# Optimization experiments

Hardware: AMD Instinct MI355X
Metric: run time of the kernel (lower is better)

The kernel has to match this reference:

```python
import jax, jax.numpy as jnp
import numpy as np
import math

B, S, H = 2, 2048, 1024
NH, DK, DV = 16, 64, 64
PAD = 0
VOCAB = 32000


def setup_inputs() -> dict:
    key = jax.random.key(0)
    ks = jax.random.split(key, 6)
    batch = jax.random.normal(ks[0], (B, S, H), dtype=jnp.float32)
    input_ids = jax.random.randint(ks[1], (B, S), 1, VOCAB)
    n_pad = S // 20
    input_ids = input_ids.at[:, S - n_pad:].set(PAD)
    init = 1.0 / math.sqrt(H)  # xavier-ish scale
    W_Q = jax.random.normal(ks[2], (H, NH * DK), dtype=jnp.float32) * init
    W_K = jax.random.normal(ks[3], (H, NH * DK), dtype=jnp.float32) * init
    W_V = jax.random.normal(ks[4], (H, NH * DV), dtype=jnp.float32) * init
    W_O = jax.random.normal(ks[5], (NH * DV, H), dtype=jnp.float32) * init
    return {
        "batch": batch, "input_ids": input_ids,
        "W_Q": W_Q, "W_K": W_K, "W_V": W_V,
        "b_Q": jnp.zeros((NH * DK,), jnp.float32),
        "b_K": jnp.zeros((NH * DK,), jnp.float32),
        "b_V": jnp.zeros((NH * DV,), jnp.float32),
        "W_O": W_O, "b_O": jnp.zeros((H,), jnp.float32),
    }


def reference(batch, input_ids, W_Q, W_K, W_V, b_Q, b_K, b_V, W_O, b_O):
    Bn, Sn, _ = batch.shape
    NEG = jnp.float32(-jnp.inf)
    # causal mask [S,S]: 0 where i>=j else -inf
    i = jnp.arange(Sn)
    causal = jnp.where(i[:, None] >= i[None, :], 0.0, NEG).astype(batch.dtype)
    # padding mask [B,1,S]: -inf at pad key positions
    pad = jnp.where(input_ids == PAD, NEG, 0.0).astype(batch.dtype)
    mask = causal[None, :, :] + pad[:, None, :]  # [B,S,S]

    Q = (batch @ W_Q + b_Q).reshape(Bn, Sn, NH, DK)
    K = (batch @ W_K + b_K).reshape(Bn, Sn, NH, DK)
    V = (batch @ W_V + b_V).reshape(Bn, Sn, NH, DV)

    scores = jnp.einsum('bqhd,bkhd->bhqk', Q, K) / math.sqrt(DK)
    attn = jax.nn.softmax(scores + mask[:, None, :, :], axis=-1)
    out = jnp.einsum('bhqk,bkhd->bqhd', attn, V).reshape(Bn, Sn, NH * DV)
    return out @ W_O + b_O
```

## Files before the change

### kernel.cpp

```cpp
#include <hip/hip_runtime.h>
#include <stdint.h>


typedef unsigned short u16;
typedef __attribute__((ext_vector_type(8))) __bf16 bf16x8;
typedef __attribute__((ext_vector_type(4))) float f32x4;
typedef __attribute__((ext_vector_type(4))) short s16x4;
typedef __attribute__((ext_vector_type(8))) short s16x8;
typedef __attribute__((ext_vector_type(2))) uint32_t u32x2;

#define SCL 0.18033688011112042f

__device__ __forceinline__ u16 f2bf(float f) {
  union { float f; uint32_t u; } v; v.f = f;
  uint32_t r = v.u + 0x7FFFu + ((v.u >> 16) & 1u);
  return (u16)(r >> 16);
}

__device__ __forceinline__ void gl_lds16(const u16* g, u16* l) {
  auto gp = reinterpret_cast<const __attribute__((address_space(1))) uint32_t*>(
      reinterpret_cast<uintptr_t>(g));
  auto lp = reinterpret_cast<__attribute__((address_space(3))) uint32_t*>(
      reinterpret_cast<uintptr_t>(l));
  __builtin_amdgcn_global_load_lds(gp, lp, 16, 0, 0);
}

__global__ void k_prologue(const float* __restrict__ batch, const int* __restrict__ ids,
                           const float* __restrict__ W_Q, const float* __restrict__ W_K,
                           const float* __restrict__ W_V, const float* __restrict__ W_O,
                           u16* __restrict__ Xbf, u16* __restrict__ dqkv, u16* __restrict__ dwo,
                           unsigned long long* __restrict__ pb) {
  __shared__ float tile[32][33];
  const int bx = blockIdx.x, t = threadIdx.x;
  if (bx < 4096) {
    int idx = (bx * 256 + t) * 4;
    const float4 v = *reinterpret_cast<const float4*>(batch + idx);
    uint2 o;
    o.x = (uint32_t)f2bf(v.x) | ((uint32_t)f2bf(v.y) << 16);
    o.y = (uint32_t)f2bf(v.z) | ((uint32_t)f2bf(v.w) << 16);
    *reinterpret_cast<uint2*>(Xbf + idx) = o;
  } else if (bx < 8192) {
    int b2 = bx - 4096;
    int z = b2 >> 10;
    b2 &= 1023;
    const float* src = z == 0 ? W_Q : (z == 1 ? W_K : (z == 2 ? W_V : W_O));
    u16* dst = z < 3 ? dqkv + (size_t)z * 1024 * 1024 : dwo;
    int c0 = (b2 & 31) * 32, r0 = (b2 >> 5) * 32;
    int tx = t & 31, ty = t >> 5;
#pragma unroll
    for (int i = 0; i < 4; ++i)
      tile[ty + i * 8][tx] = src[(size_t)(r0 + ty + i * 8) * 1024 + c0 + tx];
    __syncthreads();
#pragma unroll
    for (int i = 0; i < 4; ++i)
      dst[(size_t)(c0 + ty + i * 8) * 1024 + r0 + tx] = f2bf(tile[tx][ty + i * 8]);
  } else {
    int idx = (bx - 8192) * 4 + (t >> 6);
    int ln = t & 63;
    int b = idx >> 5, j = idx & 31;
    unsigned long long m = __ballot(ids[b * 2048 + j * 64 + ln] == 0);
    if (ln == 0) pb[idx] = m;
  }
}


__device__ __forceinline__ void gemm_tile_acc(
    const u16* __restrict__ A, const u16* __restrict__ Bt, int K,
    int tm, int tn, u16* As0, u16* As1, u16* Bs0, u16* Bs1, f32x4 acc[4][4]) {
  const int t = threadIdx.x, wv = t >> 6, ln = t & 63;
  const int wr = (wv & 1) * 64, wc = (wv >> 1) * 64;
  const int lr = ln & 15, q8 = (ln >> 4) * 8;
  const int srow = ln >> 2, scol = (ln & 3) * 8;

  for (int k0 = 0; k0 < K; k0 += 64) {
#pragma unroll
    for (int i = 0; i < 2; ++i) {
      int c = wv + i * 4;
      const size_t ra = (size_t)(tm + c * 16 + srow) * K + k0 + scol;
      const size_t rb = (size_t)(tn + c * 16 + srow) * K + k0 + scol;
      gl_lds16(A + ra,       As0 + c * 512 + ln * 8);
      gl_lds16(A + ra + 32,  As1 + c * 512 + ln * 8);
      gl_lds16(Bt + rb,      Bs0 + c * 512 + ln * 8);
      gl_lds16(Bt + rb + 32, Bs1 + c * 512 + ln * 8);
    }
    __syncthreads();
#pragma unroll
    for (int s = 0; s < 2; ++s) {
      const u16* Asb = s ? As1 : As0;
      const u16* Bsb = s ? Bs1 : Bs0;
      bf16x8 av[4], bv[4];
#pragma unroll
      for (int m = 0; m < 4; ++m)
        av[m] = *reinterpret_cast<const bf16x8*>(Asb + (wr + m * 16 + lr) * 32 + q8);
#pragma unroll
      for (int n = 0; n < 4; ++n)
        bv[n] = *reinterpret_cast<const bf16x8*>(Bsb + (wc + n * 16 + lr) * 32 + q8);
#pragma unroll
      for (int m = 0; m < 4; ++m)
#pragma unroll
        for (int n = 0; n < 4; ++n)
          acc[m][n] = __builtin_amdgcn_mfma_f32_16x16x32_bf16(av[m], bv[n], acc[m][n], 0, 0, 0);
    }
    __syncthreads();
  }
}

__global__ __launch_bounds__(256) void k_qkv(
    const u16* __restrict__ X, const u16* __restrict__ Wt,
    const float* __restrict__ bQ, const float* __restrict__ bK, const float* __restrict__ bV,
    u16* __restrict__ Qt, u16* __restrict__ Kt, u16* __restrict__ Vt) {
  __shared__ __align__(16) u16 As0[128 * 32];
  __shared__ __align__(16) u16 As1[128 * 32];
  __shared__ __align__(16) u16 Bs0[128 * 32];
  __shared__ __align__(16) u16 Bs1[128 * 32];
  f32x4 acc[4][4] = {};
  const int tm = blockIdx.x * 128, tn = blockIdx.y * 128;
  gemm_tile_acc(X, Wt, 1024, tm, tn, As0, As1, Bs0, Bs1, acc);

  const int t = threadIdx.x, wv = t >> 6, ln = t & 63;
  const int wr = (wv & 1) * 64, wc = (wv >> 1) * 64;
  const int lr = ln & 15, q4 = (ln >> 4) * 4;
  const int which = tn >> 10;

  if (which == 0) {
#pragma unroll
    for (int n = 0; n < 4; ++n) {
      int f = (tn + wc + n * 16 + lr) & 1023;
      float bb = bQ[f];
      int h = f >> 6, dd = f & 63;
      int kh = dd >> 5, qq = (dd & 31) >> 3, e = dd & 7;
#pragma unroll
      for (int m = 0; m < 4; ++m)
#pragma unroll
        for (int r = 0; r < 4; ++r) {
          int gr = tm + wr + m * 16 + q4 + r;
          int b = gr >> 11, s = gr & 2047;
          int bh = b * 16 + h;
          size_t addr = (((size_t)(bh * 64 + (s >> 5)) * 4 + ((s & 31) >> 4) * 2 + kh) << 9) +
                        ((s & 15) + 16 * qq) * 8 + e;
          Qt[addr] = f2bf((acc[m][n][r] + bb) * SCL);
        }
    }
  } else if (which == 1) {
#pragma unroll
    for (int n = 0; n < 4; ++n) {
      int f = (tn + wc + n * 16 + lr) & 1023;
      float bb = bK[f];
      int h = f >> 6, dd = f & 63;
      int kh = dd >> 5, qq = (dd & 31) >> 3, e = dd & 7;
#pragma unroll
      for (int m = 0; m < 4; ++m)
#pragma unroll
        for (int r = 0; r < 4; ++r) {
          int gr = tm + wr + m * 16 + q4 + r;
          int b = gr >> 11, s = gr & 2047;
          int bh = b * 16 + h;
          size_t addr = (((size_t)(bh * 32 + (s >> 6)) * 8 + kh * 4 + ((s & 63) >> 4)) << 9) +
                        ((s & 15) + 16 * qq) * 8 + e;
          Kt[addr] = f2bf(acc[m][n][r] + bb);
        }
    }
  } else {
#pragma unroll
    for (int n = 0; n < 4; ++n) {
      int f = (tn + wc + n * 16 + lr) & 1023;
      float bb = bV[f];
      int h = f >> 6, dd = f & 63;
      int md = dd >> 4, iv = dd & 15;
#pragma unroll
      for (int m = 0; m < 4; ++m) {
        int gr0 = tm + wr + m * 16 + q4;
        int b = gr0 >> 11, s0 = gr0 & 2047;
        int bh = b * 16 + h;
        int j = s0 >> 6, k5 = s0 & 63;
        int mp = k5 >> 5, g = (k5 & 15) >> 2, h0 = (k5 & 16) >> 2;
        size_t addr = (((size_t)(bh * 32 + j) * 8 + mp * 4 + md) << 9) +
                      (g * 16 + iv) * 8 + h0;
        uint2 pk;
        pk.x = (uint32_t)f2bf(acc[m][n][0] + bb) | ((uint32_t)f2bf(acc[m][n][1] + bb) << 16);
        pk.y = (uint32_t)f2bf(acc[m][n][2] + bb) | ((uint32_t)f2bf(acc[m][n][3] + bb) << 16);
        *reinterpret_cast<uint2*>(Vt + addr) = pk;
      }
    }
  }
}

__global__ __launch_bounds__(256) void k_out(
    const u16* __restrict__ O, const u16* __restrict__ WoT,
    const float* __restrict__ bO, float* __restrict__ out) {
  __shared__ __align__(16) u16 As0[128 * 32];
  __shared__ __align__(16) u16 As1[128 * 32];
  __shared__ __align__(16) u16 Bs0[128 * 32];
  __shared__ __align__(16) u16 Bs1[128 * 32];
  f32x4 acc[4][4] = {};
  const int tm = blockIdx.x * 128, tn = blockIdx.y * 128;
  gemm_tile_acc(O, WoT, 1024, tm, tn, As0, As1, Bs0, Bs1, acc);

  const int t = threadIdx.x, wv = t >> 6, ln = t & 63;
  const int wr = (wv & 1) * 64, wc = (wv >> 1) * 64;
  const int lr = ln & 15, q4 = (ln >> 4) * 4;
#pragma unroll
  for (int n = 0; n < 4; ++n) {
    int gc = tn + wc + n * 16 + lr;
    float bb = bO[gc];
#pragma unroll
    for (int m = 0; m < 4; ++m)
#pragma unroll
      for (int r = 0; r < 4; ++r) {
        int gr = tm + wr + m * 16 + q4 + r;
        out[(size_t)gr * 1024 + gc] = acc[m][n][r] + bb;
      }
  }
}

__global__ __launch_bounds__(256, 3) void k_attn(
    const u16* __restrict__ Qt, const u16* __restrict__ Kt, const u16* __restrict__ Vt,
    const unsigned long long* __restrict__ padbits,
    u16* __restrict__ Opart, float* __restrict__ Lpart) {
  __shared__ __align__(16) u16 KsA[2 * 4096];
  __shared__ __align__(16) u16 VsA[2 * 4096];

  const int id = blockIdx.x;
  const int bh = id & 31;
  const int w = 39 - (id >> 5);
  int p, c;
  if (w < 4)       { p = w;                    c = 0; }
  else if (w < 12) { p = 4 + ((w - 4) >> 1);   c = (w - 4) & 1; }
  else if (w < 24) { p = 8 + (w - 12) / 3;     c = (w - 12) % 3; }
  else             { p = 12 + ((w - 24) >> 2); c = (w - 24) & 3; }
  const int jts = c * 8;
  const int jte = min(2 * p + 2, jts + 8);
  const int slot = bh * 40 + w;
  const int bI = bh >> 4;

  const int t = threadIdx.x, wv = t >> 6, ln = t & 63;
  const int lr = ln & 15, q4 = (ln >> 4) * 4;
  const int qbase = p * 128 + wv * 32;
  const int qrow = wv * 32;

  bf16x8 bq[2][2];
  {
    const u16* qb = Qt + (((size_t)(bh * 64 + (qbase >> 5)) * 4) << 9) + ln * 8;
#pragma unroll
    for (int n = 0; n < 2; ++n)
#pragma unroll
      for (int kh = 0; kh < 2; ++kh)
        bq[n][kh] = *reinterpret_cast<const bf16x8*>(qb + ((n * 2 + kh) << 9));
  }

  float lo[2] = {0.f, 0.f};
  f32x4 Oc[4][2] = {};

  const int st = t * 8;
  const u16* kgp = Kt + (((size_t)(bh * 32 + jts)) << 12) + st;
  const u16* vgp = Vt + (((size_t)(bh * 32 + jts)) << 12) + st;

#pragma unroll
  for (int r = 0; r < 2; ++r) {
    gl_lds16(kgp + r * 2048, &KsA[st + r * 2048]);
    gl_lds16(vgp + r * 2048, &VsA[st + r * 2048]);
  }
  __syncthreads();

  int co = 0;
  for (int j = jts; j < jte; ++j) {
    if (j + 1 < jte) {
      kgp += 4096; vgp += 4096;
      const int no = co ^ 4096;
#pragma unroll
      for (int r = 0; r < 2; ++r) {
        gl_lds16(kgp + r * 2048, &KsA[no + st + r * 2048]);
        gl_lds16(vgp + r * 2048, &VsA[no + st + r * 2048]);
      }
    }

    const int kb = j * 64;
    const unsigned long long pb = padbits[bI * 32 + j];
    const bool masked = (kb + 63 > qbase) || (pb != 0);

    f32x4 sc[4][2] = {};
#pragma unroll
    for (int m = 0; m < 4; ++m) {
      const bf16x8 ak0 = *reinterpret_cast<const bf16x8*>(&KsA[co + m * 512 + ln * 8]);
      const bf16x8 ak1 = *reinterpret_cast<const bf16x8*>(&KsA[co + (4 + m) * 512 + ln * 8]);
#pragma unroll
      for (int n = 0; n < 2; ++n) {
        sc[m][n] = __builtin_amdgcn_mfma_f32_16x16x32_bf16(ak0, bq[n][0], sc[m][n], 0, 0, 0);
        sc[m][n] = __builtin_amdgcn_mfma_f32_16x16x32_bf16(ak1, bq[n][1], sc[m][n], 0, 0, 0);
      }
    }

    s16x4 pbf[4][2];
#pragma unroll
    for (int n = 0; n < 2; ++n) {
      if (masked) {
        const int qabs = qbase + n * 16 + lr;
#pragma unroll
        for (int m = 0; m < 4; ++m)
#pragma unroll
          for (int r = 0; r < 4; ++r) {
            const int sl = m * 16 + q4 + r;
            const bool dead = (kb + sl > qabs) || ((pb >> sl) & 1ull);
            sc[m][n][r] = dead ? -1e30f : sc[m][n][r];
          }
      }
      float ps = 0.f;
#pragma unroll
      for (int m = 0; m < 4; ++m) {
        float p0 = __builtin_amdgcn_exp2f(sc[m][n][0]);
        float p1 = __builtin_amdgcn_exp2f(sc[m][n][1]);
        float p2 = __builtin_amdgcn_exp2f(sc[m][n][2]);
        float p3 = __builtin_amdgcn_exp2f(sc[m][n][3]);
        ps += (p0 + p1) + (p2 + p3);
        u32x2 pk;
        pk.x = __builtin_amdgcn_perm(__float_as_uint(p1), __float_as_uint(p0), 0x07060302);
        pk.y = __builtin_amdgcn_perm(__float_as_uint(p3), __float_as_uint(p2), 0x07060302);
        pbf[m][n] = __builtin_bit_cast(s16x4, pk);
      }
      lo[n] += ps;
    }

#pragma unroll
    for (int mp = 0; mp < 2; ++mp)
#pragma unroll
      for (int md = 0; md < 4; ++md) {
        const s16x8 vv =
            *reinterpret_cast<const s16x8*>(&VsA[co + (mp * 4 + md) * 512 + ln * 8]);
        const s16x4 vlo = __builtin_shufflevector(vv, vv, 0, 1, 2, 3);
        const s16x4 vhi = __builtin_shufflevector(vv, vv, 4, 5, 6, 7);
#pragma unroll
        for (int n = 0; n < 2; ++n) {
          Oc[md][n] = __builtin_amdgcn_mfma_f32_16x16x16bf16_1k(
              vlo, pbf[2 * mp][n], Oc[md][n], 0, 0, 0);
          Oc[md][n] = __builtin_amdgcn_mfma_f32_16x16x16bf16_1k(
              vhi, pbf[2 * mp + 1][n], Oc[md][n], 0, 0, 0);
        }
      }

    if (j + 1 < jte) __syncthreads();
    co ^= 4096;
  }

  const size_t obase = (size_t)slot * 8192;
#pragma unroll
  for (int n = 0; n < 2; ++n) {
    lo[n] += __shfl_xor(lo[n], 16, 64);
    lo[n] += __shfl_xor(lo[n], 32, 64);
    const float inv = 1.f / lo[n];
    const int qlocal = qrow + n * 16 + lr;
#pragma unroll
    for (int md = 0; md < 4; ++md) {
      uint2 pk;
      pk.x = (uint32_t)f2bf(Oc[md][n][0] * inv) | ((uint32_t)f2bf(Oc[md][n][1] * inv) << 16);
      pk.y = (uint32_t)f2bf(Oc[md][n][2] * inv) | ((uint32_t)f2bf(Oc[md][n][3] * inv) << 16);
      *reinterpret_cast<uint2*>(Opart + obase + (size_t)qlocal * 64 + md * 16 + q4) = pk;
    }
    if (ln < 16) Lpart[slot * 128 + qlocal] = lo[n];
  }
}

__global__ __launch_bounds__(256) void k_merge(
    const u16* __restrict__ Opart, const float* __restrict__ Lpart, u16* __restrict__ O) {
  const int bh = blockIdx.x >> 5, sub = blockIdx.x & 31;
  const int p = sub >> 1, half = sub & 1;
  const int nc = p < 4 ? 1 : p < 8 ? 2 : p < 12 ? 3 : 4;
  const int pre = p < 4 ? p
               : p < 8 ? 4 + (p - 4) * 2
               : p < 12 ? 12 + (p - 8) * 3
               : 24 + (p - 12) * 4;
  const int slot0 = bh * 40 + pre;

  const int t = threadIdx.x;
  const int q = half * 64 + (t >> 2), ds = (t & 3) * 16;

  float wc[4], wsum = 0.f;
  for (int cI = 0; cI < nc; ++cI) {
    wc[cI] = Lpart[(slot0 + cI) * 128 + q];
    wsum += wc[cI];
  }
  const float inv = 1.f / wsum;

  float acc[16];
#pragma unroll
  for (int e = 0; e < 16; ++e) acc[e] = 0.f;
  for (int cI = 0; cI < nc; ++cI) {
    const u16* src = Opart + (size_t)(slot0 + cI) * 8192 + q * 64 + ds;
    uint4 a = *reinterpret_cast<const uint4*>(src);
    uint4 b = *reinterpret_cast<const uint4*>(src + 8);
    uint32_t uu[8] = {a.x, a.y, a.z, a.w, b.x, b.y, b.z, b.w};
    const float wci = wc[cI];
#pragma unroll
    for (int pp = 0; pp < 8; ++pp) {
      acc[2 * pp]     += wci * __uint_as_float(uu[pp] << 16);
      acc[2 * pp + 1] += wci * __uint_as_float(uu[pp] & 0xFFFF0000u);
    }
  }

  const int bI = bh >> 4, hI = bh & 15;
  const size_t row = (size_t)(bI * 2048 + p * 128 + q);
  u16* dst = O + row * 1024 + hI * 64 + ds;
  uint32_t op[8];
#pragma unroll
  for (int pp = 0; pp < 8; ++pp)
    op[pp] = (uint32_t)f2bf(acc[2 * pp] * inv) | ((uint32_t)f2bf(acc[2 * pp + 1] * inv) << 16);
  *reinterpret_cast<uint4*>(dst) = *reinterpret_cast<const uint4*>(&op[0]);
  *reinterpret_cast<uint4*>(dst + 8) = *reinterpret_cast<const uint4*>(&op[4]);
}


extern "C" void kernel_launch(void* const* d_in, const int* in_sizes, int n_in,
                              void* d_out, int out_size, void* d_ws, size_t ws_size,
                              hipStream_t stream) {
  (void)in_sizes; (void)n_in; (void)out_size; (void)ws_size;
  const float* batch = (const float*)d_in[0];
  const int* ids     = (const int*)d_in[1];
  const float* W_Q   = (const float*)d_in[2];
  const float* W_K   = (const float*)d_in[3];
  const float* W_V   = (const float*)d_in[4];
  const float* b_Q   = (const float*)d_in[5];
  const float* b_K   = (const float*)d_in[6];
  const float* b_V   = (const float*)d_in[7];
  const float* W_O   = (const float*)d_in[8];
  const float* b_O   = (const float*)d_in[9];
  float* out = (float*)d_out;

  u16* ws = (u16*)d_ws;
  u16* Xbf   = ws;
  u16* WqkvT = Xbf + 4194304;
  u16* WoT   = WqkvT + 3145728;
  u16* Qtb   = WoT + 1048576;
  u16* Ktb   = Qtb + 4194304;
  u16* Vtb   = Ktb + 4194304;
  u16* Opart = Vtb + 4194304;
  float* Lpart = (float*)WqkvT;
  u16* Ob    = Xbf;

  unsigned long long* padbits =
      (unsigned long long*)((char*)d_out + (size_t)out_size * 4 - 512);

  k_prologue<<<8208, 256, 0, stream>>>(batch, ids, W_Q, W_K, W_V, W_O, Xbf, WqkvT, WoT, padbits);
  k_qkv<<<dim3(32, 24), 256, 0, stream>>>(Xbf, WqkvT, b_Q, b_K, b_V, Qtb, Ktb, Vtb);
  k_attn<<<1280, 256, 0, stream>>>(Qtb, Ktb, Vtb, padbits, Opart, Lpart);
  k_merge<<<1024, 256, 0, stream>>>(Opart, Lpart, Ob);
  k_out<<<dim3(32, 8), 256, 0, stream>>>(Ob, WoT, b_O, out);
}
```

Before: 192.0 us.

## Double-buffer GEMM LDS tiles and prefetch the next K slice during MFMA

Restructures the shared GEMM mainloop used by the QKV and output projections. It previously loaded a 64-wide K chunk and then computed, with no overlap. It now walks K in 32-wide steps with two ping-pong LDS buffers, issuing async global-to-LDS loads for the next step before the MFMAs on the current one. The aim is to hide global load latency behind matrix math while keeping LDS usage the same. The cost is more loop iterations, and correctness relies on the barrier waiting for the async loads to complete.

```diff
diff --git a/kernel.cpp b/kernel.cpp
--- a/kernel.cpp
+++ b/kernel.cpp
@@ -66,42 +66,47 @@
 
 __device__ __forceinline__ void gemm_tile_acc(
     const u16* __restrict__ A, const u16* __restrict__ Bt, int K,
-    int tm, int tn, u16* As0, u16* As1, u16* Bs0, u16* Bs1, f32x4 acc[4][4]) {
+    int tm, int tn, u16* AsA, u16* BsA, f32x4 acc[4][4]) {
   const int t = threadIdx.x, wv = t >> 6, ln = t & 63;
   const int wr = (wv & 1) * 64, wc = (wv >> 1) * 64;
   const int lr = ln & 15, q8 = (ln >> 4) * 8;
   const int srow = ln >> 2, scol = (ln & 3) * 8;
 
-  for (int k0 = 0; k0 < K; k0 += 64) {
-#pragma unroll
-    for (int i = 0; i < 2; ++i) {
-      int c = wv + i * 4;
-      const size_t ra = (size_t)(tm + c * 16 + srow) * K + k0 + scol;
-      const size_t rb = (size_t)(tn + c * 16 + srow) * K + k0 + scol;
-      gl_lds16(A + ra,       As0 + c * 512 + ln * 8);
-      gl_lds16(A + ra + 32,  As1 + c * 512 + ln * 8);
-      gl_lds16(Bt + rb,      Bs0 + c * 512 + ln * 8);
-      gl_lds16(Bt + rb + 32, Bs1 + c * 512 + ln * 8);
-    }
-    __syncthreads();
-#pragma unroll
-    for (int s = 0; s < 2; ++s) {
-      const u16* Asb = s ? As1 : As0;
-      const u16* Bsb = s ? Bs1 : Bs0;
-      bf16x8 av[4], bv[4];
-#pragma unroll
-      for (int m = 0; m < 4; ++m)
-        av[m] = *reinterpret_cast<const bf16x8*>(Asb + (wr + m * 16 + lr) * 32 + q8);
+  const u16* a0 = A  + (size_t)(tm + wv * 16 + srow) * K + scol;
+  const u16* a1 = A  + (size_t)(tm + (wv + 4) * 16 + srow) * K + scol;
+  const u16* b0 = Bt + (size_t)(tn + wv * 16 + srow) * K + scol;
+  const u16* b1 = Bt + (size_t)(tn + (wv + 4) * 16 + srow) * K + scol;
+  const int l0 = wv * 512 + ln * 8, l1 = (wv + 4) * 512 + ln * 8;
+
+  gl_lds16(a0, AsA + l0);
+  gl_lds16(a1, AsA + l1);
+  gl_lds16(b0, BsA + l0);
+  gl_lds16(b1, BsA + l1);
+  __syncthreads();
+
+  int co = 0;
+  for (int k0 = 0; k0 < K; k0 += 32) {
+    if (k0 + 32 < K) {
+      const int no = co ^ 4096;
+      gl_lds16(a0 + k0 + 32, AsA + no + l0);
+      gl_lds16(a1 + k0 + 32, AsA + no + l1);
+      gl_lds16(b0 + k0 + 32, BsA + no + l0);
+      gl_lds16(b1 + k0 + 32, BsA + no + l1);
+    }
+    bf16x8 av[4], bv[4];
+#pragma unroll
+    for (int m = 0; m < 4; ++m)
+      av[m] = *reinterpret_cast<const bf16x8*>(AsA + co + (wr + m * 16 + lr) * 32 + q8);
+#pragma unroll
+    for (int n = 0; n < 4; ++n)
+      bv[n] = *reinterpret_cast<const bf16x8*>(BsA + co + (wc + n * 16 + lr) * 32 + q8);
+#pragma unroll
+    for (int m = 0; m < 4; ++m)
 #pragma unroll
       for (int n = 0; n < 4; ++n)
-        bv[n] = *reinterpret_cast<const bf16x8*>(Bsb + (wc + n * 16 + lr) * 32 + q8);
-#pragma unroll
-      for (int m = 0; m < 4; ++m)
-#pragma unroll
-        for (int n = 0; n < 4; ++n)
-          acc[m][n] = __builtin_amdgcn_mfma_f32_16x16x32_bf16(av[m], bv[n], acc[m][n], 0, 0, 0);
-    }
-    __syncthreads();
+        acc[m][n] = __builtin_amdgcn_mfma_f32_16x16x32_bf16(av[m], bv[n], acc[m][n], 0, 0, 0);
+    if (k0 + 32 < K) __syncthreads();
+    co ^= 4096;
   }
 }
 
@@ -109,13 +114,11 @@
     const u16* __restrict__ X, const u16* __restrict__ Wt,
     const float* __restrict__ bQ, const float* __restrict__ bK, const float* __restrict__ bV,
     u16* __restrict__ Qt, u16* __restrict__ Kt, u16* __restrict__ Vt) {
-  __shared__ __align__(16) u16 As0[128 * 32];
-  __shared__ __align__(16) u16 As1[128 * 32];
-  __shared__ __align__(16) u16 Bs0[128 * 32];
-  __shared__ __align__(16) u16 Bs1[128 * 32];
+  __shared__ __align__(16) u16 AsA[2 * 4096];
+  __shared__ __align__(16) u16 BsA[2 * 4096];
   f32x4 acc[4][4] = {};
   const int tm = blockIdx.x * 128, tn = blockIdx.y * 128;
-  gemm_tile_acc(X, Wt, 1024, tm, tn, As0, As1, Bs0, Bs1, acc);
+  gemm_tile_acc(X, Wt, 1024, tm, tn, AsA, BsA, acc);
 
   const int t = threadIdx.x, wv = t >> 6, ln = t & 63;
   const int wr = (wv & 1) * 64, wc = (wv >> 1) * 64;
@@ -188,13 +191,11 @@
 __global__ __launch_bounds__(256) void k_out(
     const u16* __restrict__ O, const u16* __restrict__ WoT,
     const float* __restrict__ bO, float* __restrict__ out) {
-  __shared__ __align__(16) u16 As0[128 * 32];
-  __shared__ __align__(16) u16 As1[128 * 32];
-  __shared__ __align__(16) u16 Bs0[128 * 32];
-  __shared__ __align__(16) u16 Bs1[128 * 32];
+  __shared__ __align__(16) u16 AsA[2 * 4096];
+  __shared__ __align__(16) u16 BsA[2 * 4096];
   f32x4 acc[4][4] = {};
   const int tm = blockIdx.x * 128, tn = blockIdx.y * 128;
-  gemm_tile_acc(O, WoT, 1024, tm, tn, As0, As1, Bs0, Bs1, acc);
+  gemm_tile_acc(O, WoT, 1024, tm, tn, AsA, BsA, acc);
 
   const int t = threadIdx.x, wv = t >> 6, ln = t & 63;
   const int wr = (wv & 1) * 64, wc = (wv >> 1) * 64;
```

Measured after the change: 186.9 us. -2.6%, faster.
